# Optimization experiments

Measured on AMD Instinct MI355X. Metric: run time of the kernel, lower is better.

The kernel has to match this reference:

```python
import jax, jax.numpy as jnp
import numpy as np

N_NODES = 100000
D = 128


def setup_inputs() -> dict:
    key = jax.random.key(0)
    ks = jax.random.split(key, 6)
    x = jax.random.normal(ks[0], (N_NODES, 300), dtype=jnp.float32)
    n_id = jnp.arange(N_NODES, dtype=jnp.int64)
    edge_index = jax.random.randint(ks[1], (2, 1600000), 0, N_NODES, dtype=jnp.int64)
    history = jax.random.randint(ks[2], (4096, 50), 0, N_NODES, dtype=jnp.int64)
    candidates = jax.random.randint(ks[3], (4096, 20), 0, N_NODES, dtype=jnp.int64)
    W_enc = jax.random.normal(ks[4], (300, D), dtype=jnp.float32) * 0.05
    W_gnn = jax.random.normal(ks[5], (D, D), dtype=jnp.float32) * 0.05
    return {"x": x, "n_id": n_id, "edge_index": edge_index,
            "history": history, "candidates": candidates,
            "W_enc": W_enc, "W_gnn": W_gnn}


def reference(x, n_id, edge_index, history, candidates, W_enc, W_gnn):
    N = x.shape[0]
    # news encoder: linear projection of raw node features -> [N, D]
    news_emb = x @ W_enc
    # gnn: mean aggregation over incoming edges, then linear
    src, dst = edge_index[0], edge_index[1]
    agg = jax.ops.segment_sum(news_emb[src], dst, num_segments=N)      # [N, D]
    deg = jax.ops.segment_sum(jnp.ones((src.shape[0], 1), news_emb.dtype), dst,
                              num_segments=N)                          # [N, 1]
    struct_emb = (agg / jnp.maximum(deg, 1.0)) @ W_gnn
    xx = news_emb + struct_emb                                          # [N, D]
    # scatter into dense lookup table (n_id == arange -> max_id == N, static)
    news_lookup = jnp.zeros((N, xx.shape[1]), xx.dtype).at[n_id].set(xx)
    # gather histories / candidates
    history_embs = news_lookup[history]                                 # [B, H, D]
    cand_embs = news_lookup[candidates]                                 # [B, C, D]
    mask = (history != 0).astype(xx.dtype)                              # [B, H]
    sum_embs = jnp.einsum('bhd,bh->bd', history_embs, mask)
    num_read = jnp.clip(mask.sum(axis=1, keepdims=True), 1e-9, None)
    user_vec = sum_embs / num_read                                      # [B, D]
    scores = jnp.einsum('bcd,bd->bc', cand_embs, user_vec)              # [B, C]
    return scores
```

## Files before the change

kernel.cpp:

```cpp
#include <hip/hip_runtime.h>

#define NN 100000
#define DD 128
#define KE 300
#define NE 1600000
#define NB 4096
#define HL 50
#define CL 20

#define NBUCK 1563
#define SLOT  1280
#define PBLK  250
#define EPB   6400
#define EPT   25
#define EBLK  1563

#define WTE_N 40960
#define WTG_N 16384
#define PREPB ((WTE_N + WTG_N + 255) / 256)

typedef unsigned short ushort_t;
typedef unsigned char uchar_t;
using bf16x8 = __attribute__((ext_vector_type(8))) short;
using f32x4  = __attribute__((ext_vector_type(4))) float;
using v2f    = __attribute__((ext_vector_type(2))) float;

union U4B { uint4 u; bf16x8 b; unsigned a[4]; };

__device__ __forceinline__ ushort_t f2bf(float f) {
    unsigned u = __float_as_uint(f);
    unsigned r = u + 0x7FFF + ((u >> 16) & 1);
    return (ushort_t)(r >> 16);
}
__device__ __forceinline__ float bf2f(unsigned s) {
    return __uint_as_float(s << 16);
}
__device__ __forceinline__ bf16x8 pack8(float4 a, float4 b) {
    U4B r;
    r.a[0] = (unsigned)f2bf(a.x) | ((unsigned)f2bf(a.y) << 16);
    r.a[1] = (unsigned)f2bf(a.z) | ((unsigned)f2bf(a.w) << 16);
    r.a[2] = (unsigned)f2bf(b.x) | ((unsigned)f2bf(b.y) << 16);
    r.a[3] = (unsigned)f2bf(b.z) | ((unsigned)f2bf(b.w) << 16);
    return r.b;
}

__device__ __forceinline__ bf16x8 loadA8m(const float* __restrict__ x,
                                          int row, int col, bool rowok) {
    float v[8];
#pragma unroll
    for (int j = 0; j < 8; ++j) {
        int c = col + j;
        v[j] = (rowok && c < KE) ? x[(long long)row * KE + c] : 0.f;
    }
    return pack8(make_float4(v[0], v[1], v[2], v[3]),
                 make_float4(v[4], v[5], v[6], v[7]));
}

__global__ __launch_bounds__(256) void k_prep(const int* __restrict__ ei,
                                              unsigned* __restrict__ gcur,
                                              unsigned* __restrict__ pairs,
                                              const float* __restrict__ We,
                                              const float* __restrict__ Wg,
                                              ushort_t* __restrict__ wte,
                                              ushort_t* __restrict__ wtg) {
    __shared__ unsigned sh[NBUCK], sb[NBUCK], sc[NBUCK];
    const int tid = threadIdx.x;

    if (blockIdx.x < PBLK) {
        const int eb = blockIdx.x * EPB;
        for (int i = tid; i < NBUCK; i += 256) sh[i] = 0;
        __syncthreads();

        unsigned val[EPT], bk[EPT];
#pragma unroll
        for (int l = 0; l < EPT; ++l) {
            int e = eb + l * 256 + tid;
            unsigned src = (unsigned)ei[e];
            unsigned dst = (unsigned)ei[NE + e];
            val[l] = (src << 6) | (dst & 63u);
            bk[l] = dst >> 6;
            atomicAdd(&sh[bk[l]], 1u);
        }
        __syncthreads();

        for (int i = tid; i < NBUCK; i += 256) {
            unsigned h = sh[i];
            sb[i] = (unsigned)i * SLOT + (h ? atomicAdd(&gcur[i], h) : 0u);
            sc[i] = 0;
        }
        __syncthreads();

#pragma unroll
        for (int l = 0; l < EPT; ++l) {
            unsigned b = bk[l];
            unsigned pos = sb[b] + atomicAdd(&sc[b], 1u);
            if (pos < (b + 1u) * SLOT) pairs[pos] = val[l];
        }
        return;
    }

    int i = (blockIdx.x - PBLK) * 256 + tid;
    if (i < WTE_N) {
        int j = i & 7, lane = (i >> 3) & 63, cf = (i >> 9) & 7, ch = i >> 12;
        int k = ch * 32 + (lane >> 4) * 8 + j;
        int n = cf * 16 + (lane & 15);
        wte[i] = f2bf((k < KE) ? We[k * DD + n] : 0.f);
    } else if (i < WTE_N + WTG_N) {
        int t = i - WTE_N;
        int j = t & 7, lane = (t >> 3) & 63, cf = (t >> 9) & 7, ks = t >> 12;
        int k = ks * 32 + (lane >> 4) * 8 + j;
        int n = cf * 16 + (lane & 15);
        wtg[t] = f2bf(Wg[k * DD + n]);
    }
}

__global__ __launch_bounds__(256, 1) void enc_mfma(const float* __restrict__ x,
                                                   const ushort_t* __restrict__ wtF,
                                                   ushort_t* __restrict__ news,
                                                   uchar_t* __restrict__ nf8) {
    __shared__ uchar_t f8s[64 * DD];
    const int tid = threadIdx.x;
    const int w = tid >> 6, lane = tid & 63;
    const int hl = lane & 15, kg = lane >> 4;

    bf16x8 B[10][8];
#pragma unroll
    for (int c = 0; c < 10; ++c)
#pragma unroll
        for (int cf = 0; cf < 8; ++cf)
            B[c][cf] = *(const bf16x8*)&wtF[(c * 8 + cf) * 512 + lane * 8];

    for (int tile = blockIdx.x; tile < EBLK; tile += gridDim.x) {
        const int row0 = tile * 64 + w * 16;
        const int r0 = row0 + hl;
        const bool ok0 = r0 < NN;
        const float* xr = &x[(long long)r0 * KE + kg * 8];
        const float4 fz = make_float4(0.f, 0.f, 0.f, 0.f);

        float4 ra[9][2];
        if (ok0) {
#pragma unroll
            for (int c = 0; c < 9; ++c) {
                const float4* p = (const float4*)(xr + c * 32);
                ra[c][0] = p[0];
                ra[c][1] = p[1];
            }
        } else {
#pragma unroll
            for (int c = 0; c < 9; ++c) { ra[c][0] = fz; ra[c][1] = fz; }
        }
        bf16x8 a9 = loadA8m(x, r0, 288 + kg * 8, ok0);

        f32x4 acc[8];
#pragma unroll
        for (int j = 0; j < 8; ++j) acc[j] = (f32x4)0.f;

#pragma unroll
        for (int c = 0; c < 9; ++c) {
            bf16x8 a = pack8(ra[c][0], ra[c][1]);
#pragma unroll
            for (int cf = 0; cf < 8; ++cf)
                acc[cf] = __builtin_amdgcn_mfma_f32_16x16x32_bf16(a, B[c][cf], acc[cf], 0, 0, 0);
        }
#pragma unroll
        for (int cf = 0; cf < 8; ++cf)
            acc[cf] = __builtin_amdgcn_mfma_f32_16x16x32_bf16(a9, B[9][cf], acc[cf], 0, 0, 0);

#pragma unroll
        for (int cf = 0; cf < 8; ++cf)
#pragma unroll
            for (int j = 0; j < 4; ++j) {
                int lr = w * 16 + kg * 4 + j;
                int grow = tile * 64 + lr;
                int gcol = cf * 16 + hl;
                if (grow < NN)
                    news[(long long)grow * DD + gcol] = f2bf(acc[cf][j]);
                int p = __builtin_amdgcn_cvt_pk_fp8_f32(acc[cf][j], 0.f, 0, false);
                f8s[lr * DD + gcol] = (uchar_t)(p & 0xFF);
            }
        __syncthreads();
        {
            int r = tid >> 2, boff = (tid & 3) * 32;
            int grow = tile * 64 + r;
            if (grow < NN) {
                const uint4* s = (const uint4*)&f8s[r * DD + boff];
                uint4* d = (uint4*)&nf8[(long long)grow * DD + boff];
                d[0] = s[0];
                d[1] = s[1];
            }
        }
        __syncthreads();
    }
}

__global__ __launch_bounds__(512) void k_baggnn(const unsigned* __restrict__ gcur,
                                                const unsigned* __restrict__ pairs,
                                                const uchar_t* __restrict__ nf8,
                                                const ushort_t* __restrict__ news,
                                                const ushort_t* __restrict__ wtF,
                                                ushort_t* __restrict__ xxb) {
    __shared__ unsigned srcs[SLOT];
    __shared__ unsigned hist[64], base[64], cur[64];
    __shared__ ushort_t aggs[64 * DD];
    const int tid = threadIdx.x;
    const int b = blockIdx.x;
    int cnt = (int)gcur[b];
    if (cnt > SLOT) cnt = SLOT;

    if (tid < 64) hist[tid] = 0;
    __syncthreads();
    for (int i = tid; i < cnt; i += 512)
        atomicAdd(&hist[pairs[b * SLOT + i] & 63u], 1u);
    __syncthreads();

    if (tid < 64) {
        unsigned h = hist[tid], v = h;
#pragma unroll
        for (int off = 1; off < 64; off <<= 1) {
            unsigned n = __shfl_up(v, off);
            if (tid >= off) v += n;
        }
        base[tid] = v - h;
        cur[tid]  = v - h;
    }
    __syncthreads();

    for (int i = tid; i < cnt; i += 512) {
        unsigned v = pairs[b * SLOT + i];
        srcs[atomicAdd(&cur[v & 63u], 1u)] = v >> 6;
    }
    __syncthreads();

    const int w = tid >> 6, lane = tid & 63;
    const int e = lane >> 4, l = lane & 15;
    for (int d = w; d < 64; d += 8) {
        int gd = b * 64 + d;
        if (gd >= NN) break;
        int s0 = (int)base[d], c = (int)hist[d];
        float acc[8];
#pragma unroll
        for (int j = 0; j < 8; ++j) acc[j] = 0.f;

        uint2 v = make_uint2(0u, 0u);
        if (e < c)
            v = *(const uint2*)&nf8[(long long)srcs[s0 + e] * DD + l * 8];
        for (int i = 4; i < c; i += 4) {
            uint2 vn = make_uint2(0u, 0u);
            int ii = i + e;
            if (ii < c)
                vn = *(const uint2*)&nf8[(long long)srcs[s0 + ii] * DD + l * 8];
            v2f d0 = __builtin_amdgcn_cvt_pk_f32_fp8((int)v.x, false);
            v2f d1 = __builtin_amdgcn_cvt_pk_f32_fp8((int)v.x, true);
            acc[0] += d0[0]; acc[1] += d0[1]; acc[2] += d1[0]; acc[3] += d1[1];
            d0 = __builtin_amdgcn_cvt_pk_f32_fp8((int)v.y, false);
            d1 = __builtin_amdgcn_cvt_pk_f32_fp8((int)v.y, true);
            acc[4] += d0[0]; acc[5] += d0[1]; acc[6] += d1[0]; acc[7] += d1[1];
            v = vn;
        }
        {
            v2f d0 = __builtin_amdgcn_cvt_pk_f32_fp8((int)v.x, false);
            v2f d1 = __builtin_amdgcn_cvt_pk_f32_fp8((int)v.x, true);
            acc[0] += d0[0]; acc[1] += d0[1]; acc[2] += d1[0]; acc[3] += d1[1];
            d0 = __builtin_amdgcn_cvt_pk_f32_fp8((int)v.y, false);
            d1 = __builtin_amdgcn_cvt_pk_f32_fp8((int)v.y, true);
            acc[4] += d0[0]; acc[5] += d0[1]; acc[6] += d1[0]; acc[7] += d1[1];
        }

#pragma unroll
        for (int j = 0; j < 8; ++j) {
            acc[j] += __shfl_xor(acc[j], 16);
            acc[j] += __shfl_xor(acc[j], 32);
        }
        if (e == 0) {
            uint4 o;
            o.x = (unsigned)f2bf(acc[0]) | ((unsigned)f2bf(acc[1]) << 16);
            o.y = (unsigned)f2bf(acc[2]) | ((unsigned)f2bf(acc[3]) << 16);
            o.z = (unsigned)f2bf(acc[4]) | ((unsigned)f2bf(acc[5]) << 16);
            o.w = (unsigned)f2bf(acc[6]) | ((unsigned)f2bf(acc[7]) << 16);
            *(uint4*)&aggs[d * DD + (l ^ (d & 15)) * 8] = o;
        }
    }
    __syncthreads();

    const int hl = lane & 15, kg = lane >> 4;
    const int rw = (w & 3) * 16;
    const int cfb = (w >> 2) * 4;
    U4B a[4];
#pragma unroll
    for (int ks = 0; ks < 4; ++ks)
        a[ks].u = *(const uint4*)&aggs[(rw + hl) * DD + ((ks * 4 + kg) ^ hl) * 8];

    f32x4 acc[4];
#pragma unroll
    for (int j = 0; j < 4; ++j) acc[j] = (f32x4)0.f;

#pragma unroll
    for (int ks = 0; ks < 4; ++ks) {
        const ushort_t* bp = &wtF[(ks * 8 + cfb) * 512 + lane * 8];
#pragma unroll
        for (int cf = 0; cf < 4; ++cf) {
            bf16x8 bfr = *(const bf16x8*)&bp[cf * 512];
            acc[cf] = __builtin_amdgcn_mfma_f32_16x16x32_bf16(a[ks].b, bfr, acc[cf], 0, 0, 0);
        }
    }

#pragma unroll
    for (int j = 0; j < 4; ++j) {
        int lr = rw + kg * 4 + j;
        int grow = b * 64 + lr;
        if (grow < NN) {
            float s = 1.f / fmaxf((float)hist[lr], 1.f);
#pragma unroll
            for (int cf = 0; cf < 4; ++cf) {
                int gcol = (cfb + cf) * 16 + hl;
                float nv = bf2f((unsigned)news[(long long)grow * DD + gcol]);
                xxb[(long long)grow * DD + gcol] = f2bf(nv + acc[cf][j] * s);
            }
        }
    }
}

__global__ __launch_bounds__(128) void k_user(const int* __restrict__ hist,
                                              const int* __restrict__ cand,
                                              const ushort_t* __restrict__ xxb,
                                              float* __restrict__ out) {
    __shared__ float part[2][128];
    __shared__ float cnts[2];
    __shared__ float uvs[128];
    const int b = blockIdx.x, t = threadIdx.x;
    const int w = t >> 6, lane = t & 63;

    float s0 = 0.f, s1 = 0.f, cnt = 0.f;
    for (int h = w; h < HL; h += 2) {
        int id = hist[b * HL + h];
        if (id != 0) {
            unsigned v = *(const unsigned*)&xxb[(long long)id * DD + lane * 2];
            s0 += bf2f(v & 0xFFFFu);
            s1 += bf2f(v >> 16);
            cnt += 1.f;
        }
    }
    part[w][lane * 2]     = s0;
    part[w][lane * 2 + 1] = s1;
    if (lane == 0) cnts[w] = cnt;
    __syncthreads();

    float inv = 1.f / fmaxf(cnts[0] + cnts[1], 1e-9f);
    uvs[t] = (part[0][t] + part[1][t]) * inv;
    __syncthreads();

    float2 uvp = *(const float2*)&uvs[lane * 2];
    for (int c = w; c < CL; c += 2) {
        int id = cand[b * CL + c];
        unsigned v = *(const unsigned*)&xxb[(long long)id * DD + lane * 2];
        float p = uvp.x * bf2f(v & 0xFFFFu) + uvp.y * bf2f(v >> 16);
#pragma unroll
        for (int off = 32; off >= 1; off >>= 1) p += __shfl_xor(p, off);
        if (lane == 0) out[b * CL + c] = p;
    }
}

extern "C" void kernel_launch(void* const* d_in, const int* in_sizes, int n_in,
                              void* d_out, int out_size, void* d_ws, size_t ws_size,
                              hipStream_t stream) {
    const float* x    = (const float*)d_in[0];
    const int*   ei   = (const int*)d_in[2];
    const int*   hist = (const int*)d_in[3];
    const int*   cand = (const int*)d_in[4];
    const float* Wenc = (const float*)d_in[5];
    const float* Wgnn = (const float*)d_in[6];
    float* out = (float*)d_out;

    ushort_t* news_bf = (ushort_t*)d_ws;
    ushort_t* xx_bf   = news_bf + (size_t)NN * DD;
    ushort_t* wt_enc  = xx_bf + (size_t)NN * DD;
    ushort_t* wt_gnn  = wt_enc + WTE_N;
    uchar_t*  news_f8 = (uchar_t*)(wt_gnn + WTG_N);
    unsigned* gcur    = (unsigned*)(news_f8 + (size_t)NN * DD);
    unsigned* pairs   = gcur + NBUCK;

    hipMemsetAsync(gcur, 0, NBUCK * sizeof(unsigned), stream);

    k_prep<<<PBLK + PREPB, 256, 0, stream>>>(ei, gcur, pairs, Wenc, Wgnn, wt_enc, wt_gnn);
    enc_mfma<<<256, 256, 0, stream>>>(x, wt_enc, news_bf, news_f8);
    k_baggnn<<<NBUCK, 512, 0, stream>>>(gcur, pairs, news_f8, news_bf, wt_gnn, xx_bf);
    k_user<<<NB, 128, 0, stream>>>(hist, cand, xx_bf, out);
}
```

Baseline: 153.6 us.

## Fuse edge bucketing and encoder GEMM into one launch; split fp8 conversion

Merges the edge-bucketing prep kernel and the MFMA encoder into a single launch whose blocks take different roles. The encoder blocks now build the bf16 W_enc fragments directly in 80KB of shared memory instead of a separately pre-swizzled global buffer held in registers, and the grid grows to 512 encoder blocks. The fp8 copy of news embeddings moves from the encoder epilogue into a separate streaming conversion kernel. The goal is to overlap the two front-end stages and cut register pressure, at the cost of each encoder block re-converting W_enc, LDS-sourced B operands, and an extra kernel that rereads the bf16 embeddings.

```diff
diff --git a/kernel.cpp b/kernel.cpp
--- a/kernel.cpp
+++ b/kernel.cpp
@@ -14,10 +14,11 @@
 #define EPB   6400
 #define EPT   25
 #define EBLK  1563
+#define ENCB  512
 
 #define WTE_N 40960
 #define WTG_N 16384
-#define PREPB ((WTE_N + WTG_N + 255) / 256)
+#define WTGB  ((WTG_N + 255) / 256)
 
 typedef unsigned short ushort_t;
 typedef unsigned char uchar_t;
@@ -56,17 +57,21 @@
                  make_float4(v[4], v[5], v[6], v[7]));
 }
 
-__global__ __launch_bounds__(256) void k_prep(const int* __restrict__ ei,
-                                              unsigned* __restrict__ gcur,
-                                              unsigned* __restrict__ pairs,
-                                              const float* __restrict__ We,
-                                              const float* __restrict__ Wg,
-                                              ushort_t* __restrict__ wte,
-                                              ushort_t* __restrict__ wtg) {
-    __shared__ unsigned sh[NBUCK], sb[NBUCK], sc[NBUCK];
+__global__ __launch_bounds__(256, 2) void k_front(const float* __restrict__ x,
+                                                  const float* __restrict__ We,
+                                                  const float* __restrict__ Wg,
+                                                  const int* __restrict__ ei,
+                                                  unsigned* __restrict__ gcur,
+                                                  unsigned* __restrict__ pairs,
+                                                  ushort_t* __restrict__ wtg,
+                                                  ushort_t* __restrict__ news) {
+    __shared__ __align__(16) char smem[81920];
     const int tid = threadIdx.x;
 
     if (blockIdx.x < PBLK) {
+        unsigned* sh = (unsigned*)smem;
+        unsigned* sb = sh + NBUCK;
+        unsigned* sc = sb + NBUCK;
         const int eb = blockIdx.x * EPB;
         for (int i = tid; i < NBUCK; i += 256) sh[i] = 0;
         __syncthreads();
@@ -99,38 +104,37 @@
         return;
     }
 
-    int i = (blockIdx.x - PBLK) * 256 + tid;
-    if (i < WTE_N) {
-        int j = i & 7, lane = (i >> 3) & 63, cf = (i >> 9) & 7, ch = i >> 12;
-        int k = ch * 32 + (lane >> 4) * 8 + j;
-        int n = cf * 16 + (lane & 15);
-        wte[i] = f2bf((k < KE) ? We[k * DD + n] : 0.f);
-    } else if (i < WTE_N + WTG_N) {
-        int t = i - WTE_N;
-        int j = t & 7, lane = (t >> 3) & 63, cf = (t >> 9) & 7, ks = t >> 12;
-        int k = ks * 32 + (lane >> 4) * 8 + j;
-        int n = cf * 16 + (lane & 15);
-        wtg[t] = f2bf(Wg[k * DD + n]);
-    }
-}
-
-__global__ __launch_bounds__(256, 1) void enc_mfma(const float* __restrict__ x,
-                                                   const ushort_t* __restrict__ wtF,
-                                                   ushort_t* __restrict__ news,
-                                                   uchar_t* __restrict__ nf8) {
-    __shared__ uchar_t f8s[64 * DD];
-    const int tid = threadIdx.x;
+    if (blockIdx.x >= PBLK + ENCB) {
+        int t = (blockIdx.x - PBLK - ENCB) * 256 + tid;
+        if (t < WTG_N) {
+            int j = t & 7, lane = (t >> 3) & 63, cf = (t >> 9) & 7, ks = t >> 12;
+            int k = ks * 32 + (lane >> 4) * 8 + j;
+            int n = cf * 16 + (lane & 15);
+            wtg[t] = f2bf(Wg[k * DD + n]);
+        }
+        return;
+    }
+
+    ushort_t* BsF = (ushort_t*)smem;
+
+    for (int i = tid; i < KE * DD; i += 256) {
+        float v = We[i];
+        int k = i >> 7, n = i & 127;
+        int ch = k >> 5, kr = (k >> 3) & 3, j = k & 7;
+        int cf = n >> 4, hl = n & 15;
+        BsF[((ch * 8 + cf) * 64 + kr * 16 + hl) * 8 + j] = f2bf(v);
+    }
+    for (int i = tid; i < 8 * 64 * 8; i += 256) {
+        int j = i & 7, lane = (i >> 3) & 63, cf = (i >> 9) & 7;
+        int k = 288 + ((lane >> 4) & 3) * 8 + j;
+        if (k >= KE) BsF[((9 * 8 + cf) * 64 + lane) * 8 + j] = 0;
+    }
+    __syncthreads();
+
     const int w = tid >> 6, lane = tid & 63;
     const int hl = lane & 15, kg = lane >> 4;
 
-    bf16x8 B[10][8];
-#pragma unroll
-    for (int c = 0; c < 10; ++c)
-#pragma unroll
-        for (int cf = 0; cf < 8; ++cf)
-            B[c][cf] = *(const bf16x8*)&wtF[(c * 8 + cf) * 512 + lane * 8];
-
-    for (int tile = blockIdx.x; tile < EBLK; tile += gridDim.x) {
+    for (int tile = blockIdx.x - PBLK; tile < EBLK; tile += ENCB) {
         const int row0 = tile * 64 + w * 16;
         const int r0 = row0 + hl;
         const bool ok0 = r0 < NN;
@@ -159,38 +163,43 @@
         for (int c = 0; c < 9; ++c) {
             bf16x8 a = pack8(ra[c][0], ra[c][1]);
 #pragma unroll
-            for (int cf = 0; cf < 8; ++cf)
-                acc[cf] = __builtin_amdgcn_mfma_f32_16x16x32_bf16(a, B[c][cf], acc[cf], 0, 0, 0);
-        }
+            for (int cf = 0; cf < 8; ++cf) {
+                bf16x8 bfr = *(const bf16x8*)&BsF[((c * 8 + cf) * 64 + lane) * 8];
+                acc[cf] = __builtin_amdgcn_mfma_f32_16x16x32_bf16(a, bfr, acc[cf], 0, 0, 0);
+            }
+        }
+#pragma unroll
+        for (int cf = 0; cf < 8; ++cf) {
+            bf16x8 bfr = *(const bf16x8*)&BsF[((9 * 8 + cf) * 64 + lane) * 8];
+            acc[cf] = __builtin_amdgcn_mfma_f32_16x16x32_bf16(a9, bfr, acc[cf], 0, 0, 0);
+        }
+
 #pragma unroll
         for (int cf = 0; cf < 8; ++cf)
-            acc[cf] = __builtin_amdgcn_mfma_f32_16x16x32_bf16(a9, B[9][cf], acc[cf], 0, 0, 0);
-
-#pragma unroll
-        for (int cf = 0; cf < 8; ++cf)
 #pragma unroll
             for (int j = 0; j < 4; ++j) {
-                int lr = w * 16 + kg * 4 + j;
-                int grow = tile * 64 + lr;
+                int grow = row0 + kg * 4 + j;
                 int gcol = cf * 16 + hl;
                 if (grow < NN)
                     news[(long long)grow * DD + gcol] = f2bf(acc[cf][j]);
-                int p = __builtin_amdgcn_cvt_pk_fp8_f32(acc[cf][j], 0.f, 0, false);
-                f8s[lr * DD + gcol] = (uchar_t)(p & 0xFF);
             }
-        __syncthreads();
-        {
-            int r = tid >> 2, boff = (tid & 3) * 32;
-            int grow = tile * 64 + r;
-            if (grow < NN) {
-                const uint4* s = (const uint4*)&f8s[r * DD + boff];
-                uint4* d = (uint4*)&nf8[(long long)grow * DD + boff];
-                d[0] = s[0];
-                d[1] = s[1];
-            }
-        }
-        __syncthreads();
-    }
+    }
+}
+
+__global__ __launch_bounds__(256) void k_cvt8(const ushort_t* __restrict__ nb,
+                                              uchar_t* __restrict__ n8) {
+    long long i = (long long)blockIdx.x * 256 + threadIdx.x;
+    uint4 v = *(const uint4*)&nb[i * 8];
+    float f[8];
+    f[0] = bf2f(v.x & 0xFFFFu); f[1] = bf2f(v.x >> 16);
+    f[2] = bf2f(v.y & 0xFFFFu); f[3] = bf2f(v.y >> 16);
+    f[4] = bf2f(v.z & 0xFFFFu); f[5] = bf2f(v.z >> 16);
+    f[6] = bf2f(v.w & 0xFFFFu); f[7] = bf2f(v.w >> 16);
+    int p0 = __builtin_amdgcn_cvt_pk_fp8_f32(f[0], f[1], 0, false);
+    p0     = __builtin_amdgcn_cvt_pk_fp8_f32(f[2], f[3], p0, true);
+    int p1 = __builtin_amdgcn_cvt_pk_fp8_f32(f[4], f[5], 0, false);
+    p1     = __builtin_amdgcn_cvt_pk_fp8_f32(f[6], f[7], p1, true);
+    *(uint2*)&n8[i * 8] = make_uint2((unsigned)p0, (unsigned)p1);
 }
 
 __global__ __launch_bounds__(512) void k_baggnn(const unsigned* __restrict__ gcur,
@@ -373,16 +382,16 @@
 
     ushort_t* news_bf = (ushort_t*)d_ws;
     ushort_t* xx_bf   = news_bf + (size_t)NN * DD;
-    ushort_t* wt_enc  = xx_bf + (size_t)NN * DD;
-    ushort_t* wt_gnn  = wt_enc + WTE_N;
+    ushort_t* wt_gnn  = xx_bf + (size_t)NN * DD;
     uchar_t*  news_f8 = (uchar_t*)(wt_gnn + WTG_N);
     unsigned* gcur    = (unsigned*)(news_f8 + (size_t)NN * DD);
     unsigned* pairs   = gcur + NBUCK;
 
     hipMemsetAsync(gcur, 0, NBUCK * sizeof(unsigned), stream);
 
-    k_prep<<<PBLK + PREPB, 256, 0, stream>>>(ei, gcur, pairs, Wenc, Wgnn, wt_enc, wt_gnn);
-    enc_mfma<<<256, 256, 0, stream>>>(x, wt_enc, news_bf, news_f8);
+    k_front<<<PBLK + ENCB + WTGB, 256, 0, stream>>>(x, Wenc, Wgnn, ei, gcur,
+                                                    pairs, wt_gnn, news_bf);
+    k_cvt8<<<(NN * DD / 8 + 255) / 256, 256, 0, stream>>>(news_bf, news_f8);
     k_baggnn<<<NBUCK, 512, 0, stream>>>(gcur, pairs, news_f8, news_bf, wt_gnn, xx_bf);
     k_user<<<NB, 128, 0, stream>>>(hist, cand, xx_bf, out);
 }
```

After: 215.5 us. +40.3%, slower.
